# Optimization experiments

Hardware: AMD Instinct MI355X
Metric: run time of the kernel (lower is better)

## Reference

```python
import jax, jax.numpy as jnp
import numpy as np

DT = 0.01
QSVT_DEGREE = 8


def _qsvt_chebyshev(x, coeffs):
    t_prev = jnp.ones_like(x)
    out = coeffs[0] * t_prev
    t_cur = x
    out = out + coeffs[1] * t_cur
    for i in range(2, QSVT_DEGREE + 1):
        t_next = 2.0 * x * t_cur - t_prev
        out = out + coeffs[i] * t_next
        t_prev, t_cur = t_cur, t_next
    return out


def setup_inputs() -> dict:
    key = jax.random.key(0)
    k1, k2, k3, k4 = jax.random.split(key, 4)
    B, L, D = 4, 2048, 2048
    inputs = jax.random.normal(k1, (B, L, D), dtype=jnp.float32)
    j_upper = jax.random.normal(k2, (D, D), dtype=jnp.float32) * (1.0 / np.sqrt(D))
    r_diag = jnp.full((D,), 0.01, dtype=jnp.float32)
    h_proj = jax.random.normal(k3, (D, D), dtype=jnp.float32) * (1.0 / np.sqrt(D))
    # GELU Chebyshev coefficients (degree 8)
    qsvt_coefficients = jnp.array([0.5, 0.5, 0.0, -0.044, 0.0, 0.0028, 0.0, -0.0002, 0.0], dtype=jnp.float32)
    return {"inputs": inputs, "j_upper": j_upper, "r_diag": r_diag,
            "h_proj": h_proj, "qsvt_coefficients": qsvt_coefficients}


def reference(inputs, j_upper, r_diag, h_proj, qsvt_coefficients):
    x = inputs  # [B, L, D]
    # --- Port-Hamiltonian step ---
    j_matrix = j_upper - j_upper.T                    # skew-symmetric [D, D]
    r = jax.nn.softplus(r_diag)                        # diagonal dissipation [D]
    grad_h = jnp.einsum('ij,blj->bli', h_proj, x)      # [B, L, D] big GEMM
    x_mean = jnp.mean(x, axis=1)                       # [B, D]
    grad_h_mean = jnp.mean(grad_h, axis=1)             # [B, D]
    # xdot = (J - R) grad_h ; R = diag(r). Per-row: grad_h_mean @ (J - R)^T
    a_t = j_matrix.T - jnp.diag(r)                     # (J - R)^T, diag symmetric
    x_evolved = x_mean + DT * (grad_h_mean @ a_t)      # [B, D]
    x = x + (x_evolved - x_mean)[:, None, :]
    # --- QSVT Chebyshev activation ---
    sq = jnp.sum(jnp.square(x), axis=-1, keepdims=True)
    x_norm = x * jax.lax.rsqrt(jnp.maximum(sq, 1e-8))  # tf.nn.l2_normalize
    x_activated = _qsvt_chebyshev(x_norm, qsvt_coefficients)
    return x + 0.1 * x_activated
```

## Files before the change

### kernel.cpp

```cpp
#include <hip/hip_runtime.h>

#define BB 4
#define LL 2048
#define DD 2048
#define DTC 0.01f

__global__ __launch_bounds__(256) void k_mean_partial(
        const float* __restrict__ x, float* __restrict__ xsum) {
    const int CH = 16;
    int b  = blockIdx.z;
    int l0 = blockIdx.x * CH;
    int d0 = (blockIdx.y * 256 + threadIdx.x) << 2;
    const float* p = x + ((size_t)(b * LL + l0)) * DD + d0;

    float4 acc = {0.f, 0.f, 0.f, 0.f};
#pragma unroll
    for (int l = 0; l < CH; l++) {
        float4 v = *(const float4*)(p + (size_t)l * DD);
        acc.x += v.x; acc.y += v.y; acc.z += v.z; acc.w += v.w;
    }
    float* dst = xsum + b * DD + d0;
    atomicAdd(dst + 0, acc.x);
    atomicAdd(dst + 1, acc.y);
    atomicAdd(dst + 2, acc.z);
    atomicAdd(dst + 3, acc.w);
}

__global__ __launch_bounds__(256) void k_gm(
        const float* __restrict__ hproj,
        const float* __restrict__ xsum, float* __restrict__ gm) {
    int i = blockIdx.x;
    int wave = threadIdx.x >> 6, lane = threadIdx.x & 63;
    int j0 = wave * 512 + lane * 8;
    const float* row = hproj + (size_t)i * DD;

    float4 h0 = *(const float4*)(row + j0);
    float4 h1 = *(const float4*)(row + j0 + 4);
    float acc[BB];
#pragma unroll
    for (int b = 0; b < BB; b++) {
        float4 xa = *(const float4*)(xsum + b * DD + j0);
        float4 xb = *(const float4*)(xsum + b * DD + j0 + 4);
        acc[b] = h0.x*xa.x + h0.y*xa.y + h0.z*xa.z + h0.w*xa.w
               + h1.x*xb.x + h1.y*xb.y + h1.z*xb.z + h1.w*xb.w;
    }
#pragma unroll
    for (int b = 0; b < BB; b++) {
#pragma unroll
        for (int off = 32; off > 0; off >>= 1) acc[b] += __shfl_down(acc[b], off);
    }
    __shared__ float s[4][BB];
    if (lane == 0) {
#pragma unroll
        for (int b = 0; b < BB; b++) s[wave][b] = acc[b];
    }
    __syncthreads();
    if (threadIdx.x < BB) {
        int b = threadIdx.x;
        float t = s[0][b] + s[1][b] + s[2][b] + s[3][b];
        gm[b * DD + i] = t * (1.0f / LL);
    }
}

__global__ __launch_bounds__(256) void k_delta_row(
        const float* __restrict__ jup,
        const float* __restrict__ rdiag,
        const float* __restrict__ gm, float* __restrict__ delta) {
    int i = blockIdx.x;
    int wave = threadIdx.x >> 6, lane = threadIdx.x & 63;
    int j0 = wave * 512 + lane * 8;
    const float* row = jup + (size_t)i * DD;

    float4 h0 = *(const float4*)(row + j0);
    float4 h1 = *(const float4*)(row + j0 + 4);
    float acc[BB];
#pragma unroll
    for (int b = 0; b < BB; b++) {
        float4 ga = *(const float4*)(gm + b * DD + j0);
        float4 gb = *(const float4*)(gm + b * DD + j0 + 4);
        acc[b] = h0.x*ga.x + h0.y*ga.y + h0.z*ga.z + h0.w*ga.w
               + h1.x*gb.x + h1.y*gb.y + h1.z*gb.z + h1.w*gb.w;
    }
#pragma unroll
    for (int b = 0; b < BB; b++) {
#pragma unroll
        for (int off = 32; off > 0; off >>= 1) acc[b] += __shfl_down(acc[b], off);
    }
    __shared__ float s[4][BB];
    if (lane == 0) {
#pragma unroll
        for (int b = 0; b < BB; b++) s[wave][b] = acc[b];
    }
    __syncthreads();
    if (threadIdx.x < BB) {
        int b = threadIdx.x;
        float r = log1pf(expf(rdiag[i]));
        float t = s[0][b] + s[1][b] + s[2][b] + s[3][b];
        delta[b * DD + i] = DTC * (t - gm[b * DD + i] * r);
    }
}

__global__ __launch_bounds__(256) void k_delta_col(
        const float* __restrict__ jup,
        const float* __restrict__ gm, float* __restrict__ delta) {
    const int JT = 16;
    int i  = blockIdx.x * 256 + threadIdx.x;
    int j0 = blockIdx.y * JT;

    float acc[BB] = {0.f, 0.f, 0.f, 0.f};
#pragma unroll
    for (int jj = 0; jj < JT; jj++) {
        float v = jup[(size_t)(j0 + jj) * DD + i];
#pragma unroll
        for (int b = 0; b < BB; b++)
            acc[b] += gm[b * DD + j0 + jj] * v;
    }
#pragma unroll
    for (int b = 0; b < BB; b++) atomicAdd(delta + b * DD + i, -DTC * acc[b]);
}

__global__ __launch_bounds__(256) void k_main(
        const float* __restrict__ x,
        const float* __restrict__ delta,
        const float* __restrict__ coeffs,
        float* __restrict__ out) {
    int row = blockIdx.x;
    int b   = row >> 11;
    int d0  = threadIdx.x << 3;
    size_t base = (size_t)row * DD + d0;

    float4 va = *(const float4*)(x + base);
    float4 vb = *(const float4*)(x + base + 4);
    const float* dl = delta + b * DD + d0;
    float4 da = *(const float4*)dl;
    float4 db = *(const float4*)(dl + 4);
    float xv[8] = {va.x + da.x, va.y + da.y, va.z + da.z, va.w + da.w,
                   vb.x + db.x, vb.y + db.y, vb.z + db.z, vb.w + db.w};

    float ss = 0.f;
#pragma unroll
    for (int k = 0; k < 8; k++) ss += xv[k] * xv[k];
#pragma unroll
    for (int off = 32; off > 0; off >>= 1) ss += __shfl_down(ss, off);
    __shared__ float sred[4];
    int wid = threadIdx.x >> 6, lane = threadIdx.x & 63;
    if (lane == 0) sred[wid] = ss;
    __syncthreads();
    float total = sred[0] + sred[1] + sred[2] + sred[3];
    float rinv = rsqrtf(fmaxf(total, 1e-8f));

    float c[9];
#pragma unroll
    for (int k = 0; k < 9; k++) c[k] = coeffs[k];

    float o[8];
#pragma unroll
    for (int k = 0; k < 8; k++) {
        float xn = xv[k] * rinv;
        float tp = 1.0f, tc = xn;
        float r = c[0] + c[1] * xn;
#pragma unroll
        for (int n = 2; n <= 8; n++) {
            float tn = 2.0f * xn * tc - tp;
            r += c[n] * tn;
            tp = tc; tc = tn;
        }
        o[k] = xv[k] + 0.1f * r;
    }
    float4 oa = {o[0], o[1], o[2], o[3]};
    float4 ob = {o[4], o[5], o[6], o[7]};
    *(float4*)(out + base)     = oa;
    *(float4*)(out + base + 4) = ob;
}

extern "C" void kernel_launch(void* const* d_in, const int* in_sizes, int n_in,
                              void* d_out, int out_size, void* d_ws, size_t ws_size,
                              hipStream_t stream) {
    (void)in_sizes; (void)n_in; (void)out_size; (void)ws_size;
    const float* x      = (const float*)d_in[0];
    const float* jup    = (const float*)d_in[1];
    const float* rdiag  = (const float*)d_in[2];
    const float* hproj  = (const float*)d_in[3];
    const float* coeffs = (const float*)d_in[4];
    float* out = (float*)d_out;

    float* ws    = (float*)d_ws;
    float* xsum  = ws;
    float* gm    = ws + BB * DD;
    float* delta = ws + 2 * BB * DD;

    hipMemsetAsync(d_ws, 0, (size_t)(BB * DD) * sizeof(float), stream);

    k_mean_partial<<<dim3(LL / 16, DD / 1024, BB), 256, 0, stream>>>(x, xsum);
    k_gm<<<DD, 256, 0, stream>>>(hproj, xsum, gm);
    k_delta_row<<<DD, 256, 0, stream>>>(jup, rdiag, gm, delta);
    k_delta_col<<<dim3(DD / 256, DD / 16), 256, 0, stream>>>(jup, gm, delta);
    k_main<<<BB * LL, 256, 0, stream>>>(x, delta, coeffs, out);
}
```

Measured before the change: 195.8 us.

## Split mean reduction into two stages and merge delta row/col kernels

Replaces the atomic-heavy column-sum kernel with a two-stage reduction: per-chunk partial sums are written to workspace, then a small second kernel sums 32 chunks each and does far fewer atomics. The row and column parts of the delta computation are merged into one launch by block-index dispatch, both accumulating into a zeroed delta buffer via atomics. This cuts atomic contention and one kernel launch, at the cost of an extra partial-sum buffer pass and a larger memset.

Result: faster. 178.6 us (-8.8%).

```diff
diff --git a/kernel.cpp b/kernel.cpp
--- a/kernel.cpp
+++ b/kernel.cpp
@@ -4,19 +4,35 @@
 #define LL 2048
 #define DD 2048
 #define DTC 0.01f
-
-__global__ __launch_bounds__(256) void k_mean_partial(
-        const float* __restrict__ x, float* __restrict__ xsum) {
-    const int CH = 16;
+#define NCHUNK 256
+#define CH 8
+
+__global__ __launch_bounds__(256) void k_mean_stage1(
+        const float* __restrict__ x, float* __restrict__ partial) {
+    int c  = blockIdx.x;
     int b  = blockIdx.z;
-    int l0 = blockIdx.x * CH;
-    int d0 = (blockIdx.y * 256 + threadIdx.x) << 2;
+    int l0 = c * CH;
+    int d0 = blockIdx.y * 1024 + (threadIdx.x << 2);
     const float* p = x + ((size_t)(b * LL + l0)) * DD + d0;
 
     float4 acc = {0.f, 0.f, 0.f, 0.f};
 #pragma unroll
     for (int l = 0; l < CH; l++) {
         float4 v = *(const float4*)(p + (size_t)l * DD);
+        acc.x += v.x; acc.y += v.y; acc.z += v.z; acc.w += v.w;
+    }
+    *(float4*)(partial + ((size_t)(c * BB + b)) * DD + d0) = acc;
+}
+
+__global__ __launch_bounds__(256) void k_mean_stage2(
+        const float* __restrict__ partial, float* __restrict__ xsum) {
+    int d0   = blockIdx.x * 1024 + (threadIdx.x << 2);
+    int b    = blockIdx.y;
+    int c0   = blockIdx.z * 32;
+    float4 acc = {0.f, 0.f, 0.f, 0.f};
+#pragma unroll
+    for (int cc = 0; cc < 32; cc++) {
+        float4 v = *(const float4*)(partial + ((size_t)((c0 + cc) * BB + b)) * DD + d0);
         acc.x += v.x; acc.y += v.y; acc.z += v.z; acc.w += v.w;
     }
     float* dst = xsum + b * DD + d0;
@@ -62,61 +78,60 @@
     }
 }
 
-__global__ __launch_bounds__(256) void k_delta_row(
+__global__ __launch_bounds__(256) void k_delta(
         const float* __restrict__ jup,
         const float* __restrict__ rdiag,
         const float* __restrict__ gm, float* __restrict__ delta) {
-    int i = blockIdx.x;
-    int wave = threadIdx.x >> 6, lane = threadIdx.x & 63;
-    int j0 = wave * 512 + lane * 8;
-    const float* row = jup + (size_t)i * DD;
-
-    float4 h0 = *(const float4*)(row + j0);
-    float4 h1 = *(const float4*)(row + j0 + 4);
-    float acc[BB];
-#pragma unroll
-    for (int b = 0; b < BB; b++) {
-        float4 ga = *(const float4*)(gm + b * DD + j0);
-        float4 gb = *(const float4*)(gm + b * DD + j0 + 4);
-        acc[b] = h0.x*ga.x + h0.y*ga.y + h0.z*ga.z + h0.w*ga.w
-               + h1.x*gb.x + h1.y*gb.y + h1.z*gb.z + h1.w*gb.w;
-    }
-#pragma unroll
-    for (int b = 0; b < BB; b++) {
-#pragma unroll
-        for (int off = 32; off > 0; off >>= 1) acc[b] += __shfl_down(acc[b], off);
-    }
-    __shared__ float s[4][BB];
-    if (lane == 0) {
-#pragma unroll
-        for (int b = 0; b < BB; b++) s[wave][b] = acc[b];
-    }
-    __syncthreads();
-    if (threadIdx.x < BB) {
-        int b = threadIdx.x;
-        float r = log1pf(expf(rdiag[i]));
-        float t = s[0][b] + s[1][b] + s[2][b] + s[3][b];
-        delta[b * DD + i] = DTC * (t - gm[b * DD + i] * r);
-    }
-}
-
-__global__ __launch_bounds__(256) void k_delta_col(
-        const float* __restrict__ jup,
-        const float* __restrict__ gm, float* __restrict__ delta) {
-    const int JT = 16;
-    int i  = blockIdx.x * 256 + threadIdx.x;
-    int j0 = blockIdx.y * JT;
-
-    float acc[BB] = {0.f, 0.f, 0.f, 0.f};
-#pragma unroll
-    for (int jj = 0; jj < JT; jj++) {
-        float v = jup[(size_t)(j0 + jj) * DD + i];
-#pragma unroll
-        for (int b = 0; b < BB; b++)
-            acc[b] += gm[b * DD + j0 + jj] * v;
-    }
-#pragma unroll
-    for (int b = 0; b < BB; b++) atomicAdd(delta + b * DD + i, -DTC * acc[b]);
+    if (blockIdx.x < DD) {
+        int i = blockIdx.x;
+        int wave = threadIdx.x >> 6, lane = threadIdx.x & 63;
+        int j0 = wave * 512 + lane * 8;
+        const float* row = jup + (size_t)i * DD;
+
+        float4 h0 = *(const float4*)(row + j0);
+        float4 h1 = *(const float4*)(row + j0 + 4);
+        float acc[BB];
+#pragma unroll
+        for (int b = 0; b < BB; b++) {
+            float4 ga = *(const float4*)(gm + b * DD + j0);
+            float4 gb = *(const float4*)(gm + b * DD + j0 + 4);
+            acc[b] = h0.x*ga.x + h0.y*ga.y + h0.z*ga.z + h0.w*ga.w
+                   + h1.x*gb.x + h1.y*gb.y + h1.z*gb.z + h1.w*gb.w;
+        }
+#pragma unroll
+        for (int b = 0; b < BB; b++) {
+#pragma unroll
+            for (int off = 32; off > 0; off >>= 1) acc[b] += __shfl_down(acc[b], off);
+        }
+        __shared__ float s[4][BB];
+        if (lane == 0) {
+#pragma unroll
+            for (int b = 0; b < BB; b++) s[wave][b] = acc[b];
+        }
+        __syncthreads();
+        if (threadIdx.x < BB) {
+            int b = threadIdx.x;
+            float r = log1pf(expf(rdiag[i]));
+            float t = s[0][b] + s[1][b] + s[2][b] + s[3][b];
+            atomicAdd(delta + b * DD + i, DTC * (t - gm[b * DD + i] * r));
+        }
+    } else {
+        const int JT = 16;
+        int cidx = blockIdx.x - DD;
+        int i  = (cidx & 7) * 256 + threadIdx.x;
+        int j0 = (cidx >> 3) * JT;
+
+        float acc[BB] = {0.f, 0.f, 0.f, 0.f};
+#pragma unroll
+        for (int jj = 0; jj < JT; jj++) {
+            float v = jup[(size_t)(j0 + jj) * DD + i];
+#pragma unroll
+            for (int b = 0; b < BB; b++)
+                acc[b] += gm[b * DD + j0 + jj] * v;
+        }
+#pragma unroll
+        for (int b = 0; b < BB; b++) atomicAdd(delta + b * DD + i, -DTC * acc[b]);
+    }
 }
 
 __global__ __launch_bounds__(256) void k_main(
@@ -184,16 +199,17 @@
     const float* coeffs = (const float*)d_in[4];
     float* out = (float*)d_out;
 
-    float* ws    = (float*)d_ws;
-    float* xsum  = ws;
-    float* gm    = ws + BB * DD;
-    float* delta = ws + 2 * BB * DD;
-
-    hipMemsetAsync(d_ws, 0, (size_t)(BB * DD) * sizeof(float), stream);
-
-    k_mean_partial<<<dim3(LL / 16, DD / 1024, BB), 256, 0, stream>>>(x, xsum);
+    float* ws      = (float*)d_ws;
+    float* xsum    = ws;
+    float* delta   = ws + BB * DD;
+    float* gm      = ws + 2 * BB * DD;
+    float* partial = ws + 3 * BB * DD;
+
+    hipMemsetAsync(d_ws, 0, (size_t)(2 * BB * DD) * sizeof(float), stream);
+
+    k_mean_stage1<<<dim3(NCHUNK, 2, BB), 256, 0, stream>>>(x, partial);
+    k_mean_stage2<<<dim3(2, BB, 8), 256, 0, stream>>>(partial, xsum);
     k_gm<<<DD, 256, 0, stream>>>(hproj, xsum, gm);
-    k_delta_row<<<DD, 256, 0, stream>>>(jup, rdiag, gm, delta);
-    k_delta_col<<<dim3(DD / 256, DD / 16), 256, 0, stream>>>(jup, gm, delta);
+    k_delta<<<DD + DD / 2, 256, 0, stream>>>(jup, rdiag, gm, delta);
     k_main<<<BB * LL, 256, 0, stream>>>(x, delta, coeffs, out);
 }
```
